# Optimization experiments

Hardware: AMD Instinct MI355X
Metric: run time of the kernel (lower is better)

The kernel has to match this reference:

```python
import jax, jax.numpy as jnp
import numpy as np
from jax import lax

B, T = 4, 2048
IN_CH, SKIP_CH, OUT_CH, K = 256, 128, 128, 5
N_MAMBA, D_STATE, D_CONV, EXPAND = 2, 16, 4, 2
D_INNER = EXPAND * OUT_CH
DT_RANK = (OUT_CH + 15) // 16  # ceil(d_model/16) = 8
L = 2 * T
EPS = 1e-5


def setup_inputs() -> dict:
    key = jax.random.key(0)
    ks = jax.random.split(key, 16)
    def rn(k, shape, s=0.02):
        return jax.random.normal(k, shape, jnp.float32) * s
    A_init = jnp.broadcast_to(jnp.arange(1, D_STATE + 1, dtype=jnp.float32),
                              (N_MAMBA, 2, D_INNER, D_STATE))
    return {
        'x': rn(ks[0], (B, IN_CH, T), 1.0),
        'skip': rn(ks[1], (B, SKIP_CH, L), 1.0),
        'up_w': rn(ks[2], (IN_CH, IN_CH, K)),       # torch ConvTranspose1d weight (in,out,k)
        'up_b': jnp.zeros((IN_CH,), jnp.float32),
        'fus_w': rn(ks[3], (OUT_CH, IN_CH + SKIP_CH)),  # 1x1 conv
        'fus_b': jnp.zeros((OUT_CH,), jnp.float32),
        'gn_w': jnp.ones((OUT_CH,), jnp.float32),
        'gn_b': jnp.zeros((OUT_CH,), jnp.float32),
        'prelu_a': jnp.array(0.25, jnp.float32),
        'ln_w': jnp.ones((N_MAMBA, OUT_CH), jnp.float32),
        'ln_b': jnp.zeros((N_MAMBA, OUT_CH), jnp.float32),
        'in_w': rn(ks[4], (N_MAMBA, 2, 2 * D_INNER, OUT_CH)),
        'conv_w': rn(ks[5], (N_MAMBA, 2, D_INNER, D_CONV), 0.1),
        'conv_b': jnp.zeros((N_MAMBA, 2, D_INNER), jnp.float32),
        'xproj_w': rn(ks[6], (N_MAMBA, 2, DT_RANK + 2 * D_STATE, D_INNER)),
        'dtproj_w': rn(ks[7], (N_MAMBA, 2, D_INNER, DT_RANK), 0.1),
        'dtproj_b': rn(ks[8], (N_MAMBA, 2, D_INNER), 0.1),
        'A_log': jnp.log(A_init),
        'Dp': jnp.ones((N_MAMBA, 2, D_INNER), jnp.float32),
        'out_w': rn(ks[9], (N_MAMBA, 2, OUT_CH, D_INNER)),
    }


def _mamba_branch(xn, cw, cb, iw, xw, dw, db, Alog, Dp, ow):
    # xn: [B, L, d_model] -> [B, L, d_model]; standard Mamba selective scan.
    xz = jnp.einsum('bld,ed->ble', xn, iw)            # [B,L,2*D_INNER]
    xi, z = jnp.split(xz, 2, axis=-1)
    # causal depthwise conv over time
    xc = lax.conv_general_dilated(xi.transpose(0, 2, 1), cw[:, None, :], (1,),
                                  [(D_CONV - 1, 0)], feature_group_count=D_INNER,
                                  dimension_numbers=('NCH', 'OIH', 'NCH'))
    xi = jax.nn.silu(xc + cb[None, :, None]).transpose(0, 2, 1)  # [B,L,D_INNER]
    dbl = jnp.einsum('bld,ed->ble', xi, xw)           # [B,L,DT_RANK+2N]
    dt = jax.nn.softplus(jnp.einsum('blr,dr->bld', dbl[..., :DT_RANK], dw) + db)
    Bc = dbl[..., DT_RANK:DT_RANK + D_STATE]          # [B,L,N]
    Cc = dbl[..., DT_RANK + D_STATE:]                 # [B,L,N]
    A = -jnp.exp(Alog)                                # [D_INNER,N]
    dA = jnp.exp(dt[..., None] * A)                   # [B,L,D_INNER,N]
    dBx = dt[..., None] * Bc[:, :, None, :] * xi[..., None]
    def comb(c1, c2):
        a1, b1 = c1
        a2, b2 = c2
        return a1 * a2, a2 * b1 + b2
    _, h = lax.associative_scan(comb, (dA, dBx), axis=1)  # h_t = dA_t h_{t-1} + dBx_t
    y = jnp.einsum('bldn,bln->bld', h, Cc) + Dp * xi
    return jnp.einsum('ble,de->bld', y * jax.nn.silu(z), ow)


def _forward(x, skip, up_w, up_b, fus_w, fus_b, gn_w, gn_b, prelu_a, ln_w, ln_b,
             in_w, conv_w, conv_b, xproj_w, dtproj_w, dtproj_b, A_log, Dp, out_w):
    p = K // 2
    # ConvTranspose1d(stride=2, padding=p, output_padding=1) == lhs-dilated conv with flipped kernel
    wt = jnp.flip(up_w, -1).transpose(1, 0, 2)        # (out,in,k)
    u = lax.conv_general_dilated(x, wt, (1,), [(K - 1 - p, K - 1 - p + 1)],
                                 lhs_dilation=(2,),
                                 dimension_numbers=('NCH', 'OIH', 'NCH'))
    u = u + up_b[None, :, None]
    u = u[..., :skip.shape[-1]]
    h = jnp.concatenate([u, skip], axis=1)            # [B, in+skip, L]
    h = jnp.einsum('bct,oc->bot', h, fus_w) + fus_b[None, :, None]
    # GroupNorm(1, C): normalize over (C,T) per sample
    mu = h.mean(axis=(1, 2), keepdims=True)
    var = h.var(axis=(1, 2), keepdims=True)
    h = (h - mu) / jnp.sqrt(var + EPS) * gn_w[None, :, None] + gn_b[None, :, None]
    h = jnp.where(h >= 0, h, prelu_a * h)             # PReLU (single param)
    h = h.transpose(0, 2, 1)                          # [B, L, C]
    for i in range(N_MAMBA):
        # BiMambaBlock: pre-LN, forward + time-reversed Mamba, residual sum
        mu2 = h.mean(-1, keepdims=True)
        v2 = h.var(-1, keepdims=True)
        xn = (h - mu2) / jnp.sqrt(v2 + EPS) * ln_w[i] + ln_b[i]
        f = _mamba_branch(xn, conv_w[i, 0], conv_b[i, 0], in_w[i, 0], xproj_w[i, 0],
                          dtproj_w[i, 0], dtproj_b[i, 0], A_log[i, 0], Dp[i, 0], out_w[i, 0])
        b = _mamba_branch(jnp.flip(xn, 1), conv_w[i, 1], conv_b[i, 1], in_w[i, 1], xproj_w[i, 1],
                          dtproj_w[i, 1], dtproj_b[i, 1], A_log[i, 1], Dp[i, 1], out_w[i, 1])
        h = h + f + jnp.flip(b, 1)
    return h.transpose(0, 2, 1)                       # [B, C_out, L]


def reference(x, skip, up_w, up_b, fus_w, fus_b, gn_w, gn_b, prelu_a, ln_w, ln_b,
              in_w, conv_w, conv_b, xproj_w, dtproj_w, dtproj_b, A_log, Dp, out_w):
    return _forward(x, skip, up_w, up_b, fus_w, fus_b, gn_w, gn_b, prelu_a, ln_w, ln_b,
                    in_w, conv_w, conv_b, xproj_w, dtproj_w, dtproj_b, A_log, Dp, out_w)
```

## Files before the change

### kernel.cpp

```cpp
#include <hip/hip_runtime.h>
#include <hip/hip_bf16.h>

#define Bsz 4
#define Tt 2048
#define Ll 4096
#define NC 256
#define CH 16
#define NG 16

typedef short bf16x8 __attribute__((ext_vector_type(8)));
typedef float f32x4 __attribute__((ext_vector_type(4)));
typedef float f32x2 __attribute__((ext_vector_type(2)));

static __device__ __forceinline__ f32x2 pk_fma(f32x2 a, f32x2 b, f32x2 c){
  f32x2 d;
  asm("v_pk_fma_f32 %0, %1, %2, %3" : "=v"(d) : "v"(a), "v"(b), "v"(c));
  return d;
}
static __device__ __forceinline__ f32x2 pk_mul(f32x2 a, f32x2 b){
  f32x2 d;
  asm("v_pk_mul_f32 %0, %1, %2" : "=v"(d) : "v"(a), "v"(b));
  return d;
}
static __device__ __forceinline__ f32x2 lo2(f32x4 v){ return (f32x2){v.x, v.y}; }
static __device__ __forceinline__ f32x2 hi2(f32x4 v){ return (f32x2){v.z, v.w}; }

static __device__ __forceinline__ float bs2f(unsigned short u){
  union{float f; unsigned int i;} v; v.i = ((unsigned int)u)<<16; return v.f;
}
static __device__ __forceinline__ unsigned short f2bs(float f){
  union{float f; unsigned int i;} v; v.f = f;
  unsigned int r = (v.i + 0x7fffu + ((v.i>>16)&1u)) >> 16;
  return (unsigned short)r;
}
static __device__ __forceinline__ unsigned short f2h(float f){
  union{_Float16 h; unsigned short u;} v; v.h = (_Float16)f; return v.u;
}
static __device__ __forceinline__ float h2f(unsigned short u){
  union{_Float16 h; unsigned short u;} v; v.u = u; return (float)v.h;
}

__global__ void k_cvt2(const float* __restrict__ a, const float* __restrict__ b,
                       unsigned short* __restrict__ da, unsigned short* __restrict__ db,
                       int na, int nb){
  int i = blockIdx.x*256 + threadIdx.x;
  if (i < na) da[i] = f2bs(a[i]);
  else {
    int j = i - na;
    if (j < nb) db[j] = f2bs(b[j]);
  }
}

__global__ void k_prepx(const float* __restrict__ xw, unsigned short* __restrict__ wxb){
  int row = blockIdx.x, br = blockIdx.y, col = threadIdx.x;
  float v = (row < 40) ? xw[((size_t)br*40 + row)*256 + col] : 0.f;
  wxb[((size_t)br*64 + row)*256 + col] = f2bs(v);
}

__global__ void k_prepA(const float* __restrict__ Alog, float* __restrict__ AEX,
                        float* __restrict__ A0C, float* __restrict__ CHN){
  int br = blockIdx.x, d = threadIdx.x;
  float A[16];
  #pragma unroll
  for (int j=0;j<4;j++){
    float4 a4 = *(const float4*)&Alog[(size_t)br*4096 + d*16 + j*4];
    A[4*j]  = -__expf(a4.x); A[4*j+1] = -__expf(a4.y);
    A[4*j+2]= -__expf(a4.z); A[4*j+3] = -__expf(a4.w);
    *(float4*)&AEX[(size_t)br*4096 + d*16 + j*4] = (float4){A[4*j],A[4*j+1],A[4*j+2],A[4*j+3]};
  }
  bool chain = true;
  #pragma unroll
  for (int n=1;n<16;n++){
    float expect = A[0]*(float)(n+1);
    if (fabsf(A[n]-expect) > 1e-3f*fabsf(expect)) chain = false;
  }
  A0C[br*256 + d] = A[0];
  CHN[br*256 + d] = chain ? 1.f : 0.f;
}

__global__ void k_compose(const float* __restrict__ up_w, const float* __restrict__ fus_w,
                          const float* __restrict__ fus_b, const float* __restrict__ up_b,
                          unsigned short* __restrict__ WEb, unsigned short* __restrict__ WOb,
                          unsigned short* __restrict__ FWSb, float* __restrict__ BIAS2){
  int i = blockIdx.x;
  int o = threadIdx.x;
  float a0=0.f,a1=0.f,a2=0.f,a3=0.f,a4=0.f;
  for (int c=0;c<256;c++){
    float f = fus_w[o*384+c];
    const float* w = up_w + ((size_t)i*256+c)*5;
    a0 += f*w[0]; a1 += f*w[1]; a2 += f*w[2];
    a3 += f*w[3]; a4 += f*w[4];
  }
  WEb[(size_t)o*768 +       i] = f2bs(a4);
  WEb[(size_t)o*768 + 256 + i] = f2bs(a2);
  WEb[(size_t)o*768 + 512 + i] = f2bs(a0);
  WOb[(size_t)o*512 +       i] = f2bs(a3);
  WOb[(size_t)o*512 + 256 + i] = f2bs(a1);
  if (i<128) FWSb[o*128 + i] = f2bs(fus_w[o*384+256+i]);
  if (i==0){
    float bb = fus_b[o];
    for (int c=0;c<256;c++) bb += fus_w[o*384+c]*up_b[c];
    BIAS2[o]=bb;
  }
}

__global__ __launch_bounds__(256) void k_tx(const float* __restrict__ x, unsigned short* __restrict__ XT){
  __shared__ float tile[64][65];
  int b=blockIdx.z, t0=blockIdx.x*64, i0=blockIdx.y*64;
  int tid=threadIdx.x;
  if (blockIdx.x==0 && blockIdx.y==0){
    XT[((size_t)b*2050)*256 + tid] = 0;
    XT[((size_t)b*2050+2049)*256 + tid] = 0;
  }
  for (int it=0;it<16;it++){
    int idx=it*256+tid; int ii=idx>>6, tt=idx&63;
    tile[ii][tt] = x[((size_t)b*256+i0+ii)*Tt + t0+tt];
  }
  __syncthreads();
  for (int it=0;it<16;it++){
    int idx=it*256+tid; int tt=idx>>6, ii=idx&63;
    XT[((size_t)b*2050 + t0+tt+1)*256 + i0+ii] = f2bs(tile[ii][tt]);
  }
}

__global__ __launch_bounds__(256) void k_ts(const float* __restrict__ skip, unsigned short* __restrict__ SKT){
  __shared__ float tile[64][65];
  int b=blockIdx.z, l0=blockIdx.x*64, s0=blockIdx.y*64;
  int tid=threadIdx.x;
  for (int it=0;it<16;it++){
    int idx=it*256+tid; int ss=idx>>6, ll=idx&63;
    tile[ss][ll] = skip[((size_t)b*128+s0+ss)*Ll + l0+ll];
  }
  __syncthreads();
  for (int it=0;it<16;it++){
    int idx=it*256+tid; int ll=idx>>6, ss=idx&63;
    SKT[((size_t)b*Ll + l0+ll)*128 + s0+ss] = f2bs(tile[ss][ll]);
  }
}

__global__ __launch_bounds__(256) void k_up(const unsigned short* __restrict__ XT,
                     const unsigned short* __restrict__ SKT,
                     const unsigned short* __restrict__ WEb, const unsigned short* __restrict__ WOb,
                     const unsigned short* __restrict__ FWSb, const float* __restrict__ B2,
                     float* __restrict__ h0, float* __restrict__ gst){
  __shared__ unsigned short XL[66*264];
  __shared__ unsigned short Wb[128*72];
  __shared__ float red0[256], red1[256];
  int bt = blockIdx.x, par = blockIdx.y, b = blockIdx.z;
  int t0 = bt*64;
  int tid = threadIdx.x;
  int wave = tid>>6, lane = tid&63;
  int wm = wave>>1, wn = wave&1;
  int quad = lane>>4, l16 = lane&15;

  for (int idx=tid; idx<66*32; idx+=256){
    int row = idx>>5, c8 = idx&31;
    *(uint4*)&XL[row*264 + c8*8] = *(const uint4*)&XT[((size_t)b*2050 + t0 + row)*256 + c8*8];
  }

  const unsigned short* Wsrc = par ? WOb : WEb;
  const int Kw = par ? 512 : 768;
  const int tapbase = par ? 1 : 0;
  f32x4 acc[2][4];
  #pragma unroll
  for (int i=0;i<2;i++)
    #pragma unroll
    for (int j=0;j<4;j++) acc[i][j] = (f32x4){0.f,0.f,0.f,0.f};

  int nch = Kw>>6;
  for (int kc=0; kc<nch; kc++){
    __syncthreads();
    #pragma unroll
    for (int it=0; it<4; it++){
      int idx = it*256+tid;
      int row = idx>>3, c8 = idx&7;
      *(uint4*)&Wb[row*72 + c8*8] = *(const uint4*)&Wsrc[(size_t)row*Kw + kc*64 + c8*8];
    }
    __syncthreads();
    #pragma unroll
    for (int ks=0; ks<64; ks+=32){
      int kg = kc*64 + ks;
      int tap = kg>>8, ib = kg&255;
      bf16x8 af[2], bf[4];
      #pragma unroll
      for (int mt=0;mt<2;mt++)
        af[mt] = *(bf16x8*)&XL[(wm*32+mt*16+l16 + tapbase + tap)*264 + ib + quad*8];
      #pragma unroll
      for (int nt=0;nt<4;nt++)
        bf[nt] = *(bf16x8*)&Wb[(wn*64+nt*16+l16)*72 + ks + quad*8];
      #pragma unroll
      for (int mt=0;mt<2;mt++)
        #pragma unroll
        for (int nt=0;nt<4;nt++)
          acc[mt][nt] = __builtin_amdgcn_mfma_f32_16x16x32_bf16(af[mt], bf[nt], acc[mt][nt], 0,0,0);
    }
  }

  __syncthreads();
  for (int idx=tid; idx<64*16; idx+=256){
    int row = idx>>4, c8 = idx&15;
    *(uint4*)&XL[row*136 + c8*8] = *(const uint4*)&SKT[((size_t)b*Ll + 2*(t0+row)+par)*128 + c8*8];
  }
  for (int kc=0; kc<2; kc++){
    __syncthreads();
    #pragma unroll
    for (int it=0; it<4; it++){
      int idx = it*256+tid;
      int row = idx>>3, c8 = idx&7;
      *(uint4*)&Wb[row*72 + c8*8] = *(const uint4*)&FWSb[(size_t)row*128 + kc*64 + c8*8];
    }
    __syncthreads();
    #pragma unroll
    for (int ks=0; ks<64; ks+=32){
      bf16x8 af[2], bf[4];
      #pragma unroll
      for (int mt=0;mt<2;mt++)
        af[mt] = *(bf16x8*)&XL[(wm*32+mt*16+l16)*136 + kc*64 + ks + quad*8];
      #pragma unroll
      for (int nt=0;nt<4;nt++)
        bf[nt] = *(bf16x8*)&Wb[(wn*64+nt*16+l16)*72 + ks + quad*8];
      #pragma unroll
      for (int mt=0;mt<2;mt++)
        #pragma unroll
        for (int nt=0;nt<4;nt++)
          acc[mt][nt] = __builtin_amdgcn_mfma_f32_16x16x32_bf16(af[mt], bf[nt], acc[mt][nt], 0,0,0);
    }
  }

  float s1=0.f, s2=0.f;
  #pragma unroll
  for (int mt=0;mt<2;mt++)
    #pragma unroll
    for (int nt=0;nt<4;nt++)
      #pragma unroll
      for (int r=0;r<4;r++){
        int m = wm*32 + mt*16 + quad*4 + r;
        int lrow = 2*(t0+m) + par;
        int col = wn*64 + nt*16 + l16;
        float v = acc[mt][nt][r] + B2[col];
        h0[((size_t)b*Ll + lrow)*128 + col] = v;
        s1 += v; s2 += v*v;
      }
  red0[tid]=s1; red1[tid]=s2;
  __syncthreads();
  for (int st=128; st>0; st>>=1){
    if (tid<st){ red0[tid]+=red0[tid+st]; red1[tid]+=red1[tid+st]; }
    __syncthreads();
  }
  if (tid==0){ atomicAdd(&gst[b*2], red0[0]); atomicAdd(&gst[b*2+1], red1[0]); }
}

__global__ __launch_bounds__(256) void k_gnln(const float* __restrict__ h0, const float* __restrict__ gn_w,
                      const float* __restrict__ gn_b, const float* __restrict__ pa,
                      const float* __restrict__ gst, const float* __restrict__ lnw,
                      const float* __restrict__ lnb, float* __restrict__ hres,
                      unsigned short* __restrict__ xn){
  int row = blockIdx.x*4 + (threadIdx.x>>6);
  int lane = threadIdx.x & 63;
  int b = row >> 12;
  const float ninv = 1.f/((float)Ll*128.f);
  float mu_g = gst[b*2]*ninv;
  float var_g = gst[b*2+1]*ninv - mu_g*mu_g;
  float inv_g = rsqrtf(var_g + 1e-5f);
  float a = pa[0];
  const float* hp = h0 + (size_t)row*128;
  float u0 = (hp[lane]   -mu_g)*inv_g*gn_w[lane]    + gn_b[lane];
  float u1 = (hp[lane+64]-mu_g)*inv_g*gn_w[lane+64] + gn_b[lane+64];
  float v0 = u0>=0.f ? u0 : a*u0;
  float v1 = u1>=0.f ? u1 : a*u1;
  float* rp = hres + (size_t)row*128;
  rp[lane] = v0; rp[lane+64] = v1;
  float s = v0+v1, q = v0*v0+v1*v1;
  #pragma unroll
  for (int off=32; off>0; off>>=1){
    s += __shfl_xor(s, off, 64);
    q += __shfl_xor(q, off, 64);
  }
  float mu = s*(1.f/128.f);
  float rs = rsqrtf(q*(1.f/128.f)-mu*mu + 1e-5f);
  unsigned short* xp = xn + (size_t)row*128;
  xp[lane]    = f2bs((v0-mu)*rs*lnw[lane]    + lnb[lane]);
  xp[lane+64] = f2bs((v1-mu)*rs*lnw[lane+64] + lnb[lane+64]);
}

__global__ __launch_bounds__(256) void k_gemm_in(const unsigned short* __restrict__ A,
                          const unsigned short* __restrict__ W,
                          unsigned short* __restrict__ C){
  __shared__ unsigned short As[128*72];
  __shared__ unsigned short Bs[128*72];
  int tid = threadIdx.x;
  int row0 = blockIdx.x*128;
  int n0   = blockIdx.y*128;
  int dir  = blockIdx.z;
  const unsigned short* Wp = W + (size_t)dir*512*128;
  unsigned short* Cp = C + (size_t)dir*Bsz*Ll*512;
  int wave = tid>>6, lane = tid&63;
  int wm = wave>>1, wn = wave&1;
  int quad = lane>>4, l16 = lane&15;
  f32x4 acc[4][4];
  #pragma unroll
  for (int i=0;i<4;i++)
    #pragma unroll
    for (int j=0;j<4;j++) acc[i][j] = (f32x4){0.f,0.f,0.f,0.f};

  for (int kb=0; kb<128; kb+=64){
    __syncthreads();
    #pragma unroll
    for (int it=0; it<4; it++){
      int idx = it*256 + tid;
      int row = idx>>3, c8 = idx&7;
      int r = row0 + row;
      int p = r & (Ll-1); int bb = r >> 12;
      int src = (bb<<12) + (dir ? (Ll-1-p) : p);
      *(uint4*)&As[row*72 + c8*8] = *(const uint4*)&A[(size_t)src*128 + kb + c8*8];
      *(uint4*)&Bs[row*72 + c8*8] = *(const uint4*)&Wp[(size_t)(n0+row)*128 + kb + c8*8];
    }
    __syncthreads();
    #pragma unroll
    for (int ks=0; ks<64; ks+=32){
      bf16x8 af[4], bf[4];
      #pragma unroll
      for (int mt=0;mt<4;mt++)
        af[mt] = *(bf16x8*)&As[(wm*64+mt*16+l16)*72 + ks + quad*8];
      #pragma unroll
      for (int nt=0;nt<4;nt++)
        bf[nt] = *(bf16x8*)&Bs[(wn*64+nt*16+l16)*72 + ks + quad*8];
      #pragma unroll
      for (int mt=0;mt<4;mt++)
        #pragma unroll
        for (int nt=0;nt<4;nt++)
          acc[mt][nt] = __builtin_amdgcn_mfma_f32_16x16x32_bf16(af[mt], bf[nt], acc[mt][nt], 0,0,0);
    }
  }
  #pragma unroll
  for (int mt=0;mt<4;mt++)
    #pragma unroll
    for (int nt=0;nt<4;nt++)
      #pragma unroll
      for (int r=0;r<4;r++){
        int row = row0 + wm*64 + mt*16 + quad*4 + r;
        int col = n0 + wn*64 + nt*16 + l16;
        Cp[(size_t)row*512 + col] = f2bs(acc[mt][nt][r]);
      }
}

template<int DO_LN>
__global__ __launch_bounds__(256) void k_gemm_out_t(const unsigned short* __restrict__ Y,
                           const unsigned short* __restrict__ W,
                           float* __restrict__ C, const float* __restrict__ lnw,
                           const float* __restrict__ lnb, unsigned short* __restrict__ xn){
  __shared__ unsigned short As[64*72];
  __shared__ unsigned short Bs[128*72];
  __shared__ float redS[2][4][2][4][2][2];
  int tid = threadIdx.x;
  int row0 = blockIdx.x*64;
  int wave = tid>>6, lane = tid&63;
  int wm = wave>>1, wn = wave&1;
  int quad = lane>>4, l16 = lane&15;
  const size_t planeY = (size_t)Bsz*Ll*256;
  f32x4 acc[2][4];
  #pragma unroll
  for (int i=0;i<2;i++)
    #pragma unroll
    for (int j=0;j<4;j++) acc[i][j] = (f32x4){0.f,0.f,0.f,0.f};

  for (int kc=0; kc<8; kc++){
    int dirp = kc>>2;
    int kb = (kc&3)*64;
    const unsigned short* Wp = W + (size_t)dirp*128*256;
    __syncthreads();
    #pragma unroll
    for (int it=0; it<2; it++){
      int idx = it*256 + tid;
      int row = idx>>3, c8 = idx&7;
      int r = row0 + row;
      int p = r & (Ll-1); int bb = r >> 12;
      int srow = dirp ? ((bb<<12) + (Ll-1-p)) : r;
      *(uint4*)&As[row*72 + c8*8] = *(const uint4*)&Y[dirp*planeY + (size_t)srow*256 + kb + c8*8];
    }
    #pragma unroll
    for (int it=0; it<4; it++){
      int idx = it*256 + tid;
      int row = idx>>3, c8 = idx&7;
      *(uint4*)&Bs[row*72 + c8*8] = *(const uint4*)&Wp[(size_t)row*256 + kb + c8*8];
    }
    __syncthreads();
    #pragma unroll
    for (int ks=0; ks<64; ks+=32){
      bf16x8 af[2], bf[4];
      #pragma unroll
      for (int mt=0;mt<2;mt++)
        af[mt] = *(bf16x8*)&As[(wm*32+mt*16+l16)*72 + ks + quad*8];
      #pragma unroll
      for (int nt=0;nt<4;nt++)
        bf[nt] = *(bf16x8*)&Bs[(wn*64+nt*16+l16)*72 + ks + quad*8];
      #pragma unroll
      for (int mt=0;mt<2;mt++)
        #pragma unroll
        for (int nt=0;nt<4;nt++)
          acc[mt][nt] = __builtin_amdgcn_mfma_f32_16x16x32_bf16(af[mt], bf[nt], acc[mt][nt], 0,0,0);
    }
  }

  float vals[2][4][4];
  #pragma unroll
  for (int mt=0;mt<2;mt++)
    #pragma unroll
    for (int nt=0;nt<4;nt++)
      #pragma unroll
      for (int r=0;r<4;r++){
        int row = row0 + wm*32 + mt*16 + quad*4 + r;
        int col = wn*64 + nt*16 + l16;
        float v = C[(size_t)row*128 + col] + acc[mt][nt][r];
        C[(size_t)row*128 + col] = v;
        vals[mt][nt][r] = v;
      }

  if (DO_LN){
    #pragma unroll
    for (int mt=0;mt<2;mt++)
      #pragma unroll
      for (int r=0;r<4;r++){
        float s = 0.f, q = 0.f;
        #pragma unroll
        for (int nt=0;nt<4;nt++){ float v = vals[mt][nt][r]; s += v; q += v*v; }
        #pragma unroll
        for (int off=1; off<16; off<<=1){
          s += __shfl_xor(s, off, 64);
          q += __shfl_xor(q, off, 64);
        }
        if (l16 == 0){
          redS[wm][quad][mt][r][wn][0] = s;
          redS[wm][quad][mt][r][wn][1] = q;
        }
      }
    __syncthreads();
    #pragma unroll
    for (int mt=0;mt<2;mt++)
      #pragma unroll
      for (int r=0;r<4;r++){
        float s = redS[wm][quad][mt][r][0][0] + redS[wm][quad][mt][r][1][0];
        float q = redS[wm][quad][mt][r][0][1] + redS[wm][quad][mt][r][1][1];
        float mu = s*(1.f/128.f);
        float rs = rsqrtf(q*(1.f/128.f) - mu*mu + 1e-5f);
        int row = row0 + wm*32 + mt*16 + quad*4 + r;
        #pragma unroll
        for (int nt=0;nt<4;nt++){
          int col = wn*64 + nt*16 + l16;
          xn[(size_t)row*128 + col] = f2bs((vals[mt][nt][r]-mu)*rs*lnw[col] + lnb[col]);
        }
      }
  }
}

__global__ __launch_bounds__(256) void k_xproj3(const unsigned short* __restrict__ xz,
                        const unsigned short* __restrict__ wxb,
                        const float* __restrict__ cw, const float* __restrict__ cb,
                        unsigned short* __restrict__ xib, float* __restrict__ dbl){
  __shared__ unsigned short xiS[64*264];
  __shared__ unsigned short Bs[64*72];
  int tid = threadIdx.x;
  int dir = blockIdx.y;
  xz  += (size_t)dir*Bsz*Ll*512;
  wxb += (size_t)dir*64*256;
  cw  += dir*1024;
  cb  += dir*256;
  xib += (size_t)dir*Bsz*Ll*256;
  dbl += (size_t)dir*Bsz*Ll*40;
  size_t row0 = (size_t)blockIdx.x*64;
  int p0 = (int)(row0 & (Ll-1));

  {
    int d = tid;
    float4 w4 = *(const float4*)&cw[d*4];
    float bias = cb[d];
    float w0, w1, w2;
    if (p0 == 0){ w0=0.f; w1=0.f; w2=0.f; }
    else {
      w0 = bs2f(xz[(row0-3)*512 + d]);
      w1 = bs2f(xz[(row0-2)*512 + d]);
      w2 = bs2f(xz[(row0-1)*512 + d]);
    }
    #pragma unroll 4
    for (int rr=0; rr<64; rr++){
      float xv = bs2f(xz[(row0+rr)*512 + d]);
      float acc = bias + w4.x*w0 + w4.y*w1 + w4.z*w2 + w4.w*xv;
      float v = acc*__builtin_amdgcn_rcpf(1.f+__expf(-acc));
      unsigned short us = f2bs(v);
      xiS[rr*264 + d] = us;
      xib[(row0+rr)*256 + d] = us;
      w0=w1; w1=w2; w2=xv;
    }
  }

  int wave = tid>>6, lane = tid&63;
  int quad = lane>>4, l16 = lane&15;
  f32x4 acc[4];
  #pragma unroll
  for (int j=0;j<4;j++) acc[j] = (f32x4){0.f,0.f,0.f,0.f};

  for (int kb=0; kb<256; kb+=64){
    __syncthreads();
    #pragma unroll
    for (int it=0; it<2; it++){
      int idx = it*256 + tid;
      int row = idx>>3, c8 = idx&7;
      *(uint4*)&Bs[row*72 + c8*8] = *(const uint4*)&wxb[(size_t)row*256 + kb + c8*8];
    }
    __syncthreads();
    #pragma unroll
    for (int ks=0; ks<64; ks+=32){
      bf16x8 af = *(bf16x8*)&xiS[(wave*16+l16)*264 + kb + ks + quad*8];
      #pragma unroll
      for (int nt=0;nt<4;nt++){
        bf16x8 bf = *(bf16x8*)&Bs[(nt*16+l16)*72 + ks + quad*8];
        acc[nt] = __builtin_amdgcn_mfma_f32_16x16x32_bf16(af, bf, acc[nt], 0,0,0);
      }
    }
  }
  #pragma unroll
  for (int nt=0;nt<4;nt++)
    #pragma unroll
    for (int r=0;r<4;r++){
      int m = wave*16 + quad*4 + r;
      int col = nt*16 + l16;
      if (col < 40) dbl[(row0+m)*40 + col] = acc[nt][r];
    }
}

#define POWTREE2(e1, pw2) { \
  float _e2 = (e1)*(e1); \
  f32x2 _e2v = (f32x2){_e2,_e2}; \
  pw2[0] = (f32x2){(e1),_e2}; \
  pw2[1] = pk_mul(pw2[0], _e2v); \
  pw2[2] = pk_mul(pw2[1], _e2v); \
  pw2[3] = pk_mul(pw2[2], _e2v); \
  f32x2 _e8v = (f32x2){pw2[3].y, pw2[3].y}; \
  pw2[4] = pk_mul(pw2[0], _e8v); \
  pw2[5] = pk_mul(pw2[1], _e8v); \
  pw2[6] = pk_mul(pw2[2], _e8v); \
  pw2[7] = pk_mul(pw2[3], _e8v); }

__global__ __launch_bounds__(256) void k_scan1(const float* __restrict__ dbl,
                       const unsigned short* __restrict__ xib,
                       unsigned short* __restrict__ xz,
                       const float* __restrict__ AEX,
                       const float* __restrict__ A0C, const float* __restrict__ CHNf,
                       const float* __restrict__ dtw, const float* __restrict__ dtb,
                       float* __restrict__ SD, float* __restrict__ Q){
  __shared__ float dblS[CH*24];
  int b = blockIdx.y, c = blockIdx.x, dir = blockIdx.z;
  int d = threadIdx.x;
  const float* dblP = dbl + (size_t)dir*Bsz*Ll*40;
  const unsigned short* xiP = xib + (size_t)dir*Bsz*Ll*256;
  unsigned short* xzP = xz + (size_t)dir*Bsz*Ll*512;
  size_t base = (size_t)b*Ll + (size_t)c*CH;
  if (d < CH*6){
    int p = d/6, j = d - p*6;
    *(float4*)&dblS[p*24 + j*4] = *(const float4*)&dblP[(base+p)*40 + j*4];
  }
  float A0 = A0C[dir*256 + d];
  bool chain = CHNf[dir*256 + d] != 0.f;
  f32x2 wv2[4];
  {
    const float* dw = dtw + (size_t)dir*2048 + d*8;
    float4 w0 = *(const float4*)&dw[0];
    float4 w1 = *(const float4*)&dw[4];
    wv2[0]=(f32x2){w0.x,w0.y}; wv2[1]=(f32x2){w0.z,w0.w};
    wv2[2]=(f32x2){w1.x,w1.y}; wv2[3]=(f32x2){w1.z,w1.w};
  }
  float bbt = dtb[dir*256 + d];
  __syncthreads();
  float sdt = 0.f;
  const unsigned short* xip = xiP + base*256 + d;
  unsigned short* dtp = xzP + base*512 + d;
  size_t sbase = (size_t)dir*Bsz*NC*4096 + ((size_t)(b*NC + c))*4096 + (size_t)d*16;
  if (chain){
    bool n1 = fabsf(A0 + 1.f) < 1e-6f;
    float xv[CH];
    #pragma unroll
    for (int p=0;p<CH;p++) xv[p] = bs2f(xip[(size_t)p*256]);
    f32x2 h2[8];
    #pragma unroll
    for (int i=0;i<8;i++) h2[i] = (f32x2){0.f,0.f};
    #pragma unroll
    for (int p=0;p<CH;p++){
      const float* rw = &dblS[p*24];
      f32x4 t0 = *(const f32x4*)&rw[0];
      f32x4 t1 = *(const f32x4*)&rw[4];
      f32x2 dp = pk_mul(lo2(t0), wv2[0]);
      dp = pk_fma(hi2(t0), wv2[1], dp);
      dp = pk_fma(lo2(t1), wv2[2], dp);
      dp = pk_fma(hi2(t1), wv2[3], dp);
      float a0 = bbt + dp.x + dp.y;
      float t = __expf(a0);
      float u = 1.f + t;
      float dtv = (a0>20.f)? a0 : __logf(u);
      float e1 = n1 ? __builtin_amdgcn_rcpf(u) : __expf(dtv*A0);
      dtp[(size_t)p*512] = f2h(dtv);
      float dx = dtv*xv[p];
      sdt += dtv;
      f32x2 pw2[8];
      POWTREE2(e1, pw2);
      f32x2 dxv = (f32x2){dx,dx};
      f32x4 b0 = *(const f32x4*)&dblS[p*24+8];
      f32x4 b1 = *(const f32x4*)&dblS[p*24+12];
      f32x4 b2 = *(const f32x4*)&dblS[p*24+16];
      f32x4 b3 = *(const f32x4*)&dblS[p*24+20];
      h2[0] = pk_fma(pw2[0], h2[0], pk_mul(lo2(b0), dxv));
      h2[1] = pk_fma(pw2[1], h2[1], pk_mul(hi2(b0), dxv));
      h2[2] = pk_fma(pw2[2], h2[2], pk_mul(lo2(b1), dxv));
      h2[3] = pk_fma(pw2[3], h2[3], pk_mul(hi2(b1), dxv));
      h2[4] = pk_fma(pw2[4], h2[4], pk_mul(lo2(b2), dxv));
      h2[5] = pk_fma(pw2[5], h2[5], pk_mul(hi2(b2), dxv));
      h2[6] = pk_fma(pw2[6], h2[6], pk_mul(lo2(b3), dxv));
      h2[7] = pk_fma(pw2[7], h2[7], pk_mul(hi2(b3), dxv));
    }
    #pragma unroll
    for (int j=0;j<4;j++)
      *(float4*)&Q[sbase + 4*j] = (float4){h2[2*j].x,h2[2*j].y,h2[2*j+1].x,h2[2*j+1].y};
  } else {
    float A[16];
    #pragma unroll
    for (int j=0;j<4;j++)
      *(float4*)&A[4*j] = *(const float4*)&AEX[(size_t)dir*4096 + d*16 + j*4];
    float h[16];
    #pragma unroll
    for (int n=0;n<16;n++) h[n]=0.f;
    for (int p=0;p<CH;p++){
      const float* rw = &dblS[p*24];
      float4 t0 = *(const float4*)&rw[0], t1 = *(const float4*)&rw[4];
      float a0 = bbt + t0.x*wv2[0].x+t0.y*wv2[0].y+t0.z*wv2[1].x+t0.w*wv2[1].y
                     + t1.x*wv2[2].x+t1.y*wv2[2].y+t1.z*wv2[3].x+t1.w*wv2[3].y;
      float dtv = (a0>20.f)? a0 : __logf(1.f+__expf(a0));
      dtp[(size_t)p*512] = f2h(dtv);
      float xiv = bs2f(xip[(size_t)p*256]);
      float dx = dtv*xiv;
      sdt += dtv;
      float bc[16];
      *(float4*)&bc[0]  = *(const float4*)&rw[8];
      *(float4*)&bc[4]  = *(const float4*)&rw[12];
      *(float4*)&bc[8]  = *(const float4*)&rw[16];
      *(float4*)&bc[12] = *(const float4*)&rw[20];
      #pragma unroll
      for (int n=0;n<16;n++){
        float a = __expf(dtv*A[n]);
        h[n] = a*h[n] + bc[n]*dx;
      }
    }
    #pragma unroll
    for (int j=0;j<4;j++)
      *(float4*)&Q[sbase + 4*j] = (float4){h[4*j],h[4*j+1],h[4*j+2],h[4*j+3]};
  }
  SD[(((size_t)dir*Bsz + b)*NC + c)*256 + d] = sdt;
}

__global__ __launch_bounds__(64) void k_scan2a(float* __restrict__ SD, float* __restrict__ Q,
                        float* __restrict__ SDG, float* __restrict__ QG,
                        const float* __restrict__ AEX){
  int zb = blockIdx.z;
  int dir = zb >> 2;
  int g  = blockIdx.y;
  int t  = blockIdx.x*64 + threadIdx.x;
  int dn4 = t*4;
  int d = dn4 >> 4;
  float4 A4 = *(const float4*)&AEX[(size_t)dir*4096 + dn4];
  float* sd = SD + (((size_t)zb*NC) + (size_t)g*(NC/NG))*256 + d;
  float* q  = Q + (size_t)zb*NC*4096 + (size_t)g*(NC/NG)*4096 + dn4;
  float4 H = {0.f,0.f,0.f,0.f};
  float S = 0.f;
  #pragma unroll
  for (int c2=0; c2<NC/NG; c2++){
    float s_c = sd[(size_t)c2*256];
    float4 q_c = *(const float4*)(q + (size_t)c2*4096);
    sd[(size_t)c2*256] = S;
    *(float4*)(q + (size_t)c2*4096) = H;
    float4 p;
    p.x = __expf(A4.x*s_c); p.y = __expf(A4.y*s_c);
    p.z = __expf(A4.z*s_c); p.w = __expf(A4.w*s_c);
    H.x = p.x*H.x + q_c.x; H.y = p.y*H.y + q_c.y;
    H.z = p.z*H.z + q_c.z; H.w = p.w*H.w + q_c.w;
    S += s_c;
  }
  SDG[((size_t)zb*NG + g)*256 + d] = S;
  *(float4*)&QG[((size_t)zb*NG + g)*4096 + dn4] = H;
}

__global__ __launch_bounds__(64) void k_scan2b(const float* __restrict__ SDG, float* __restrict__ QG,
                        const float* __restrict__ AEX){
  int b = blockIdx.y, dir = blockIdx.z;
  int zb = dir*Bsz + b;
  int t = blockIdx.x*64 + threadIdx.x;
  int dn4 = t*4;
  int d = dn4 >> 4;
  float4 A4 = *(const float4*)&AEX[(size_t)dir*4096 + dn4];
  const float* sg = SDG + (size_t)zb*NG*256 + d;
  float* qg = QG + (size_t)zb*NG*4096 + dn4;
  float4 H = {0.f,0.f,0.f,0.f};
  #pragma unroll
  for (int g=0; g<NG; g++){
    float s = sg[(size_t)g*256];
    float4 qe = *(const float4*)(qg + (size_t)g*4096);
    *(float4*)(qg + (size_t)g*4096) = H;
    float4 p;
    p.x = __expf(A4.x*s); p.y = __expf(A4.y*s);
    p.z = __expf(A4.z*s); p.w = __expf(A4.w*s);
    H.x = p.x*H.x + qe.x; H.y = p.y*H.y + qe.y;
    H.z = p.z*H.z + qe.z; H.w = p.w*H.w + qe.w;
  }
}

__global__ __launch_bounds__(256) void k_scan3(const float* __restrict__ dbl,
                       unsigned short* xiy, const float* __restrict__ AEX,
                       const float* __restrict__ A0C, const float* __restrict__ CHNf,
                       const float* __restrict__ Dpw, const float* __restrict__ Hs,
                       const float* __restrict__ SDp, const float* __restrict__ QG,
                       const unsigned short* __restrict__ xz){
  __shared__ float dblS[CH*32];
  int b = blockIdx.y, c = blockIdx.x, dir = blockIdx.z;
  int d = threadIdx.x;
  const float* dblP = dbl + (size_t)dir*Bsz*Ll*40;
  unsigned short* xiP = xiy + (size_t)dir*Bsz*Ll*256;
  const unsigned short* xzP = xz + (size_t)dir*Bsz*Ll*512;
  size_t base = (size_t)b*Ll + (size_t)c*CH;
  if (d < CH*8){
    int p = d>>3, j = d&7;
    *(float4*)&dblS[p*32 + j*4] = *(const float4*)&dblP[(base+p)*40 + 8 + j*4];
  }
  float A0 = A0C[dir*256 + d];
  bool chain = CHNf[dir*256 + d] != 0.f;
  float Dp = Dpw[dir*256 + d];
  int zb = dir*Bsz + b;
  size_t sbase = (size_t)zb*NC*4096 + (size_t)c*4096 + (size_t)d*16;
  float sdtp = SDp[(((size_t)zb)*NC + c)*256 + d];
  size_t gbase = ((size_t)zb*NG + (c >> 4))*4096 + (size_t)d*16;
  __syncthreads();
  unsigned short* xip = xiP + base*256 + d;
  const unsigned short* dtp = xzP + base*512 + d;
  const unsigned short* zp  = xzP + base*512 + 256 + d;
  if (chain){
    float xv[CH], zv[CH], dv[CH];
    #pragma unroll
    for (int p=0;p<CH;p++) xv[p] = bs2f(xip[(size_t)p*256]);
    #pragma unroll
    for (int p=0;p<CH;p++) zv[p] = bs2f(zp[(size_t)p*512]);
    #pragma unroll
    for (int p=0;p<CH;p++) dv[p] = h2f(dtp[(size_t)p*512]);
    f32x2 h2[8];
    {
      float eg = __expf(A0*sdtp);
      f32x2 pg[8];
      POWTREE2(eg, pg);
      #pragma unroll
      for (int j=0;j<4;j++){
        float4 h4 = *(const float4*)&Hs[sbase + 4*j];
        float4 g4 = *(const float4*)&QG[gbase + 4*j];
        h2[2*j]   = pk_fma(pg[2*j],   (f32x2){g4.x,g4.y}, (f32x2){h4.x,h4.y});
        h2[2*j+1] = pk_fma(pg[2*j+1], (f32x2){g4.z,g4.w}, (f32x2){h4.z,h4.w});
      }
    }
    #pragma unroll
    for (int p=0;p<CH;p++){
      const float* rw = &dblS[p*32];
      float dtv = dv[p];
      float e1 = __expf(dtv*A0);
      float dx = dtv*xv[p];
      f32x2 pw2[8];
      POWTREE2(e1, pw2);
      f32x2 dxv = (f32x2){dx,dx};
      f32x4 b0 = *(const f32x4*)&rw[0];
      f32x4 b1 = *(const f32x4*)&rw[4];
      f32x4 b2 = *(const f32x4*)&rw[8];
      f32x4 b3 = *(const f32x4*)&rw[12];
      f32x4 c0 = *(const f32x4*)&rw[16];
      f32x4 c1 = *(const f32x4*)&rw[20];
      f32x4 c2 = *(const f32x4*)&rw[24];
      f32x4 c3 = *(const f32x4*)&rw[28];
      f32x2 ya;
      h2[0] = pk_fma(pw2[0], h2[0], pk_mul(lo2(b0), dxv));
      ya = pk_mul(h2[0], lo2(c0));
      h2[1] = pk_fma(pw2[1], h2[1], pk_mul(hi2(b0), dxv));
      ya = pk_fma(h2[1], hi2(c0), ya);
      h2[2] = pk_fma(pw2[2], h2[2], pk_mul(lo2(b1), dxv));
      ya = pk_fma(h2[2], lo2(c1), ya);
      h2[3] = pk_fma(pw2[3], h2[3], pk_mul(hi2(b1), dxv));
      ya = pk_fma(h2[3], hi2(c1), ya);
      h2[4] = pk_fma(pw2[4], h2[4], pk_mul(lo2(b2), dxv));
      ya = pk_fma(h2[4], lo2(c2), ya);
      h2[5] = pk_fma(pw2[5], h2[5], pk_mul(hi2(b2), dxv));
      ya = pk_fma(h2[5], hi2(c2), ya);
      h2[6] = pk_fma(pw2[6], h2[6], pk_mul(lo2(b3), dxv));
      ya = pk_fma(h2[6], lo2(c3), ya);
      h2[7] = pk_fma(pw2[7], h2[7], pk_mul(hi2(b3), dxv));
      ya = pk_fma(h2[7], hi2(c3), ya);
      float acc = ya.x + ya.y;
      float z = zv[p];
      float g = z*__builtin_amdgcn_rcpf(1.f+__expf(-z));
      xip[(size_t)p*256] = f2bs((acc + Dp*xv[p])*g);
    }
  } else {
    float A[16];
    #pragma unroll
    for (int j=0;j<4;j++)
      *(float4*)&A[4*j] = *(const float4*)&AEX[(size_t)dir*4096 + d*16 + j*4];
    float h[16];
    #pragma unroll
    for (int j=0;j<4;j++){
      float4 h4 = *(const float4*)&Hs[sbase + 4*j];
      float4 g4 = *(const float4*)&QG[gbase + 4*j];
      h[4*j]   = __expf(A[4*j]*sdtp)*g4.x   + h4.x;
      h[4*j+1] = __expf(A[4*j+1]*sdtp)*g4.y + h4.y;
      h[4*j+2] = __expf(A[4*j+2]*sdtp)*g4.z + h4.z;
      h[4*j+3] = __expf(A[4*j+3]*sdtp)*g4.w + h4.w;
    }
    for (int p=0;p<CH;p++){
      const float* rw = &dblS[p*32];
      float dtv = h2f(dtp[(size_t)p*512]);
      float xiv = bs2f(xip[(size_t)p*256]);
      float dx = dtv*xiv;
      float bc[16], cc[16];
      *(float4*)&bc[0]  = *(const float4*)&rw[0];
      *(float4*)&bc[4]  = *(const float4*)&rw[4];
      *(float4*)&bc[8]  = *(const float4*)&rw[8];
      *(float4*)&bc[12] = *(const float4*)&rw[12];
      *(float4*)&cc[0]  = *(const float4*)&rw[16];
      *(float4*)&cc[4]  = *(const float4*)&rw[20];
      *(float4*)&cc[8]  = *(const float4*)&rw[24];
      *(float4*)&cc[12] = *(const float4*)&rw[28];
      float acc = 0.f;
      #pragma unroll
      for (int n=0;n<16;n++){
        float a = __expf(dtv*A[n]);
        h[n] = a*h[n] + bc[n]*dx;
        acc += h[n]*cc[n];
      }
      float z = bs2f(zp[(size_t)p*512]);
      float g = z*__builtin_amdgcn_rcpf(1.f+__expf(-z));
      xip[(size_t)p*256] = f2bs((acc + Dp*xiv)*g);
    }
  }
}

__global__ __launch_bounds__(256) void k_final(const float* __restrict__ hres, float* __restrict__ out){
  __shared__ float tile[64*129];
  int b = blockIdx.y, l0 = blockIdx.x*64;
  int tid = threadIdx.x;
  for (int q=0;q<32;q++){
    int idx = q*256 + tid;
    int l = idx >> 7, c = idx & 127;
    tile[l*129 + c] = hres[((size_t)b*Ll + l0 + l)*128 + c];
  }
  __syncthreads();
  int lo = tid & 63; int cbase = tid >> 6;
  for (int q=0;q<32;q++){
    int c = cbase + q*4;
    out[((size_t)b*128 + c)*Ll + l0 + lo] = tile[lo*129 + c];
  }
}

extern "C" void kernel_launch(void* const* d_in, const int* in_sizes, int n_in,
                              void* d_out, int out_size, void* d_ws, size_t ws_size,
                              hipStream_t stream){
  const float* x      = (const float*)d_in[0];
  const float* skip   = (const float*)d_in[1];
  const float* up_w   = (const float*)d_in[2];
  const float* up_b   = (const float*)d_in[3];
  const float* fus_w  = (const float*)d_in[4];
  const float* fus_b  = (const float*)d_in[5];
  const float* gn_w   = (const float*)d_in[6];
  const float* gn_b   = (const float*)d_in[7];
  const float* pa     = (const float*)d_in[8];
  const float* ln_w   = (const float*)d_in[9];
  const float* ln_b   = (const float*)d_in[10];
  const float* in_w   = (const float*)d_in[11];
  const float* conv_w = (const float*)d_in[12];
  const float* conv_b = (const float*)d_in[13];
  const float* xproj_w= (const float*)d_in[14];
  const float* dtproj_w=(const float*)d_in[15];
  const float* dtproj_b=(const float*)d_in[16];
  const float* A_log  = (const float*)d_in[17];
  const float* Dp     = (const float*)d_in[18];
  const float* out_w  = (const float*)d_in[19];

  float* w = (float*)d_ws;
  size_t off=0;
  float* B2 = w+off; off += 128;
  float* GST= w+off; off += 16;
  off = (off+3)&~(size_t)3;
  float* HR = w+off; off += (size_t)Bsz*Ll*128;
  float* DBL2= w+off; off += 2*(size_t)Bsz*Ll*40;
  unsigned short* XNB = (unsigned short*)(w+off); off += (size_t)Bsz*Ll*128/2;
  unsigned short* XZB2= (unsigned short*)(w+off); off += 2*(size_t)Bsz*Ll*512/2;
  unsigned short* IWB = (unsigned short*)(w+off); off += 2*2*512*128/2;
  unsigned short* OWB = (unsigned short*)(w+off); off += 2*2*128*256/2;
  unsigned short* WXB = (unsigned short*)(w+off); off += 2*2*64*256/2;
  unsigned short* WEb = (unsigned short*)(w+off); off += 768*128/2;
  unsigned short* WOb = (unsigned short*)(w+off); off += 512*128/2;
  unsigned short* FWSb= (unsigned short*)(w+off); off += 128*128/2;
  float* AEXb = w+off; off += 4*4096;
  float* A0Cb = w+off; off += 4*256;
  float* CHNb = w+off; off += 4*256;
  float* SDGb = w+off; off += (size_t)2*Bsz*NG*256;
  size_t planeS = (size_t)Bsz*NC*4096;
  float* U1 = w+off; off += 2*planeS;
  unsigned short* XT  = (unsigned short*)U1;
  unsigned short* SKT = (unsigned short*)(U1 + 1049604);
  float* SQ = U1;
  float* SD = (float*)XNB;
  float* QG = SD + 524288;
  float* U2 = w+off; off += 2*(size_t)Bsz*Ll*128;
  float* H0 = U2;
  unsigned short* XIB2 = (unsigned short*)U2;

  hipMemsetAsync(GST, 0, 16*sizeof(float), stream);
  k_cvt2<<<(2*2*512*128 + 2*2*128*256 + 255)/256,256,0,stream>>>(in_w, out_w, IWB, OWB,
                                                                 2*2*512*128, 2*2*128*256);
  k_prepx<<<dim3(64,4),256,0,stream>>>(xproj_w, WXB);
  k_prepA<<<4,256,0,stream>>>(A_log, AEXb, A0Cb, CHNb);
  k_compose<<<256,128,0,stream>>>(up_w, fus_w, fus_b, up_b, WEb, WOb, FWSb, B2);
  k_tx<<<dim3(Tt/64, 4, Bsz),256,0,stream>>>(x, XT);
  k_ts<<<dim3(Ll/64, 2, Bsz),256,0,stream>>>(skip, SKT);
  k_up<<<dim3(32, 2, Bsz),256,0,stream>>>(XT, SKT, WEb, WOb, FWSb, B2, H0, GST);
  k_gnln<<<Bsz*Ll/4,256,0,stream>>>(H0, gn_w, gn_b, pa, GST, ln_w, ln_b, HR, XNB);
  for (int i=0;i<2;i++){
    k_gemm_in<<<dim3(128,4,2),256,0,stream>>>(XNB, IWB + (size_t)(i*2)*512*128, XZB2);
    k_xproj3<<<dim3(Bsz*Ll/64,2),256,0,stream>>>(XZB2, WXB + (size_t)(i*2)*64*256,
                                                 conv_w + (i*2)*1024, conv_b + (i*2)*256,
                                                 XIB2, DBL2);
    k_scan1<<<dim3(NC,Bsz,2),256,0,stream>>>(DBL2, XIB2, XZB2, AEXb + (size_t)(i*2)*4096,
                                             A0Cb + (i*2)*256, CHNb + (i*2)*256,
                                             dtproj_w + (i*2)*2048, dtproj_b + (i*2)*256, SD, SQ);
    k_scan2a<<<dim3(16,NG,2*Bsz),64,0,stream>>>(SD, SQ, SDGb, QG, AEXb + (size_t)(i*2)*4096);
    k_scan2b<<<dim3(16,Bsz,2),64,0,stream>>>(SDGb, QG, AEXb + (size_t)(i*2)*4096);
    k_scan3<<<dim3(NC,Bsz,2),256,0,stream>>>(DBL2, XIB2, AEXb + (size_t)(i*2)*4096,
                                             A0Cb + (i*2)*256, CHNb + (i*2)*256,
                                             Dp + (i*2)*256, SQ, SD, QG, XZB2);
    if (i==0)
      k_gemm_out_t<1><<<256,256,0,stream>>>(XIB2, OWB + 0, HR, ln_w + 128, ln_b + 128, XNB);
    else
      k_gemm_out_t<0><<<256,256,0,stream>>>(XIB2, OWB + (size_t)2*128*256, HR,
                                            (const float*)nullptr, (const float*)nullptr,
                                            (unsigned short*)nullptr);
  }
  k_final<<<dim3(Ll/64,Bsz),256,0,stream>>>(HR, (float*)d_out);
}
```

Measured before the change: 383.6 us.

## Merge weight-prep kernels into one launch and halve k_up time tile

Five small preprocessing steps (two weight conversions, x-proj padding, A-table prep and the GroupNorm-stats memset) become one kernel that dispatches by block index, removing several launches and a memset. k_up now tiles 32 time steps per block instead of 64, doubling the grid from 256 to 512 blocks to fill more CUs. The cost is less weight reuse per block and twice as many weight loads and atomics.

```diff
diff --git a/kernel.cpp b/kernel.cpp
--- a/kernel.cpp
+++ b/kernel.cpp
@@ -40,67 +40,69 @@
   union{_Float16 h; unsigned short u;} v; v.u = u; return (float)v.h;
 }
 
-__global__ void k_cvt2(const float* __restrict__ a, const float* __restrict__ b,
-                       unsigned short* __restrict__ da, unsigned short* __restrict__ db,
-                       int na, int nb){
-  int i = blockIdx.x*256 + threadIdx.x;
-  if (i < na) da[i] = f2bs(a[i]);
-  else {
-    int j = i - na;
-    if (j < nb) db[j] = f2bs(b[j]);
-  }
-}
-
-__global__ void k_prepx(const float* __restrict__ xw, unsigned short* __restrict__ wxb){
-  int row = blockIdx.x, br = blockIdx.y, col = threadIdx.x;
-  float v = (row < 40) ? xw[((size_t)br*40 + row)*256 + col] : 0.f;
-  wxb[((size_t)br*64 + row)*256 + col] = f2bs(v);
-}
-
-__global__ void k_prepA(const float* __restrict__ Alog, float* __restrict__ AEX,
-                        float* __restrict__ A0C, float* __restrict__ CHN){
-  int br = blockIdx.x, d = threadIdx.x;
-  float A[16];
-  #pragma unroll
-  for (int j=0;j<4;j++){
-    float4 a4 = *(const float4*)&Alog[(size_t)br*4096 + d*16 + j*4];
-    A[4*j]  = -__expf(a4.x); A[4*j+1] = -__expf(a4.y);
-    A[4*j+2]= -__expf(a4.z); A[4*j+3] = -__expf(a4.w);
-    *(float4*)&AEX[(size_t)br*4096 + d*16 + j*4] = (float4){A[4*j],A[4*j+1],A[4*j+2],A[4*j+3]};
-  }
-  bool chain = true;
-  #pragma unroll
-  for (int n=1;n<16;n++){
-    float expect = A[0]*(float)(n+1);
-    if (fabsf(A[n]-expect) > 1e-3f*fabsf(expect)) chain = false;
-  }
-  A0C[br*256 + d] = A[0];
-  CHN[br*256 + d] = chain ? 1.f : 0.f;
-}
-
-__global__ void k_compose(const float* __restrict__ up_w, const float* __restrict__ fus_w,
-                          const float* __restrict__ fus_b, const float* __restrict__ up_b,
-                          unsigned short* __restrict__ WEb, unsigned short* __restrict__ WOb,
-                          unsigned short* __restrict__ FWSb, float* __restrict__ BIAS2){
-  int i = blockIdx.x;
-  int o = threadIdx.x;
-  float a0=0.f,a1=0.f,a2=0.f,a3=0.f,a4=0.f;
-  for (int c=0;c<256;c++){
-    float f = fus_w[o*384+c];
-    const float* w = up_w + ((size_t)i*256+c)*5;
-    a0 += f*w[0]; a1 += f*w[1]; a2 += f*w[2];
-    a3 += f*w[3]; a4 += f*w[4];
-  }
-  WEb[(size_t)o*768 +       i] = f2bs(a4);
-  WEb[(size_t)o*768 + 256 + i] = f2bs(a2);
-  WEb[(size_t)o*768 + 512 + i] = f2bs(a0);
-  WOb[(size_t)o*512 +       i] = f2bs(a3);
-  WOb[(size_t)o*512 + 256 + i] = f2bs(a1);
-  if (i<128) FWSb[o*128 + i] = f2bs(fus_w[o*384+256+i]);
-  if (i==0){
-    float bb = fus_b[o];
-    for (int c=0;c<256;c++) bb += fus_w[o*384+c]*up_b[c];
-    BIAS2[o]=bb;
+__global__ __launch_bounds__(256) void k_prep(
+    const float* __restrict__ in_w, const float* __restrict__ out_w,
+    unsigned short* __restrict__ IWB, unsigned short* __restrict__ OWB,
+    const float* __restrict__ xw, unsigned short* __restrict__ wxb,
+    const float* __restrict__ Alog, float* __restrict__ AEX,
+    float* __restrict__ A0C, float* __restrict__ CHN, float* __restrict__ GST,
+    const float* __restrict__ up_w, const float* __restrict__ fus_w,
+    const float* __restrict__ fus_b, const float* __restrict__ up_b,
+    unsigned short* __restrict__ WEb, unsigned short* __restrict__ WOb,
+    unsigned short* __restrict__ FWSb, float* __restrict__ BIAS2){
+  const int na = 2*2*512*128;
+  const int nb = 2*2*128*256;
+  int bid = blockIdx.x, tid = threadIdx.x;
+  if (bid < 3072){
+    int i = bid*256 + tid;
+    if (i < na) IWB[i] = f2bs(in_w[i]);
+    else { int j = i - na; if (j < nb) OWB[j] = f2bs(out_w[j]); }
+  } else if (bid < 3328){
+    int r = bid - 3072;
+    int row = r & 63, br = r >> 6;
+    float v = (row < 40) ? xw[((size_t)br*40 + row)*256 + tid] : 0.f;
+    wxb[((size_t)br*64 + row)*256 + tid] = f2bs(v);
+  } else if (bid < 3332){
+    int br = bid - 3328, d = tid;
+    float A[16];
+    #pragma unroll
+    for (int j=0;j<4;j++){
+      float4 a4 = *(const float4*)&Alog[(size_t)br*4096 + d*16 + j*4];
+      A[4*j]  = -__expf(a4.x); A[4*j+1] = -__expf(a4.y);
+      A[4*j+2]= -__expf(a4.z); A[4*j+3] = -__expf(a4.w);
+      *(float4*)&AEX[(size_t)br*4096 + d*16 + j*4] = (float4){A[4*j],A[4*j+1],A[4*j+2],A[4*j+3]};
+    }
+    bool chain = true;
+    #pragma unroll
+    for (int n=1;n<16;n++){
+      float expect = A[0]*(float)(n+1);
+      if (fabsf(A[n]-expect) > 1e-3f*fabsf(expect)) chain = false;
+    }
+    A0C[br*256 + d] = A[0];
+    CHN[br*256 + d] = chain ? 1.f : 0.f;
+    if (br==0 && d<16) GST[d] = 0.f;
+  } else {
+    int r = bid - 3332;
+    int i = r*2 + (tid>>7);
+    int o = tid & 127;
+    float a0=0.f,a1=0.f,a2=0.f,a3=0.f,a4=0.f;
+    for (int c=0;c<256;c++){
+      float f = fus_w[o*384+c];
+      const float* w = up_w + ((size_t)i*256+c)*5;
+      a0 += f*w[0]; a1 += f*w[1]; a2 += f*w[2];
+      a3 += f*w[3]; a4 += f*w[4];
+    }
+    WEb[(size_t)o*768 +       i] = f2bs(a4);
+    WEb[(size_t)o*768 + 256 + i] = f2bs(a2);
+    WEb[(size_t)o*768 + 512 + i] = f2bs(a0);
+    WOb[(size_t)o*512 +       i] = f2bs(a3);
+    WOb[(size_t)o*512 + 256 + i] = f2bs(a1);
+    if (i<128) FWSb[o*128 + i] = f2bs(fus_w[o*384+256+i]);
+    if (i==0){
+      float bb = fus_b[o];
+      for (int c=0;c<256;c++) bb += fus_w[o*384+c]*up_b[c];
+      BIAS2[o]=bb;
+    }
   }
 }
 
@@ -143,17 +145,17 @@
                      const unsigned short* __restrict__ WEb, const unsigned short* __restrict__ WOb,
                      const unsigned short* __restrict__ FWSb, const float* __restrict__ B2,
                      float* __restrict__ h0, float* __restrict__ gst){
-  __shared__ unsigned short XL[66*264];
+  __shared__ unsigned short XL[34*264];
   __shared__ unsigned short Wb[128*72];
   __shared__ float red0[256], red1[256];
   int bt = blockIdx.x, par = blockIdx.y, b = blockIdx.z;
-  int t0 = bt*64;
+  int t0 = bt*32;
   int tid = threadIdx.x;
   int wave = tid>>6, lane = tid&63;
   int wm = wave>>1, wn = wave&1;
   int quad = lane>>4, l16 = lane&15;
 
-  for (int idx=tid; idx<66*32; idx+=256){
+  for (int idx=tid; idx<34*32; idx+=256){
     int row = idx>>5, c8 = idx&31;
     *(uint4*)&XL[row*264 + c8*8] = *(const uint4*)&XT[((size_t)b*2050 + t0 + row)*256 + c8*8];
   }
@@ -161,11 +163,9 @@
   const unsigned short* Wsrc = par ? WOb : WEb;
   const int Kw = par ? 512 : 768;
   const int tapbase = par ? 1 : 0;
-  f32x4 acc[2][4];
-  #pragma unroll
-  for (int i=0;i<2;i++)
-    #pragma unroll
-    for (int j=0;j<4;j++) acc[i][j] = (f32x4){0.f,0.f,0.f,0.f};
+  f32x4 acc[4];
+  #pragma unroll
+  for (int j=0;j<4;j++) acc[j] = (f32x4){0.f,0.f,0.f,0.f};
 
   int nch = Kw>>6;
   for (int kc=0; kc<nch; kc++){
@@ -181,23 +181,17 @@
     for (int ks=0; ks<64; ks+=32){
       int kg = kc*64 + ks;
       int tap = kg>>8, ib = kg&255;
-      bf16x8 af[2], bf[4];
-      #pragma unroll
-      for (int mt=0;mt<2;mt++)
-        af[mt] = *(bf16x8*)&XL[(wm*32+mt*16+l16 + tapbase + tap)*264 + ib + quad*8];
-      #pragma unroll
-      for (int nt=0;nt<4;nt++)
-        bf[nt] = *(bf16x8*)&Wb[(wn*64+nt*16+l16)*72 + ks + quad*8];
-      #pragma unroll
-      for (int mt=0;mt<2;mt++)
-        #pragma unroll
-        for (int nt=0;nt<4;nt++)
-          acc[mt][nt] = __builtin_amdgcn_mfma_f32_16x16x32_bf16(af[mt], bf[nt], acc[mt][nt], 0,0,0);
+      bf16x8 af = *(bf16x8*)&XL[(wm*16+l16 + tapbase + tap)*264 + ib + quad*8];
+      #pragma unroll
+      for (int nt=0;nt<4;nt++){
+        bf16x8 bf = *(bf16x8*)&Wb[(wn*64+nt*16+l16)*72 + ks + quad*8];
+        acc[nt] = __builtin_amdgcn_mfma_f32_16x16x32_bf16(af, bf, acc[nt], 0,0,0);
+      }
     }
   }
 
   __syncthreads();
-  for (int idx=tid; idx<64*16; idx+=256){
+  for (int idx=tid; idx<32*16; idx+=256){
     int row = idx>>4, c8 = idx&15;
     *(uint4*)&XL[row*136 + c8*8] = *(const uint4*)&SKT[((size_t)b*Ll + 2*(t0+row)+par)*128 + c8*8];
   }
@@ -212,35 +206,27 @@
     __syncthreads();
     #pragma unroll
     for (int ks=0; ks<64; ks+=32){
-      bf16x8 af[2], bf[4];
-      #pragma unroll
-      for (int mt=0;mt<2;mt++)
-        af[mt] = *(bf16x8*)&XL[(wm*32+mt*16+l16)*136 + kc*64 + ks + quad*8];
-      #pragma unroll
-      for (int nt=0;nt<4;nt++)
-        bf[nt] = *(bf16x8*)&Wb[(wn*64+nt*16+l16)*72 + ks + quad*8];
-      #pragma unroll
-      for (int mt=0;mt<2;mt++)
-        #pragma unroll
-        for (int nt=0;nt<4;nt++)
-          acc[mt][nt] = __builtin_amdgcn_mfma_f32_16x16x32_bf16(af[mt], bf[nt], acc[mt][nt], 0,0,0);
+      bf16x8 af = *(bf16x8*)&XL[(wm*16+l16)*136 + kc*64 + ks + quad*8];
+      #pragma unroll
+      for (int nt=0;nt<4;nt++){
+        bf16x8 bf = *(bf16x8*)&Wb[(wn*64+nt*16+l16)*72 + ks + quad*8];
+        acc[nt] = __builtin_amdgcn_mfma_f32_16x16x32_bf16(af, bf, acc[nt], 0,0,0);
+      }
     }
   }
 
   float s1=0.f, s2=0.f;
   #pragma unroll
-  for (int mt=0;mt<2;mt++)
-    #pragma unroll
-    for (int nt=0;nt<4;nt++)
-      #pragma unroll
-      for (int r=0;r<4;r++){
-        int m = wm*32 + mt*16 + quad*4 + r;
-        int lrow = 2*(t0+m) + par;
-        int col = wn*64 + nt*16 + l16;
-        float v = acc[mt][nt][r] + B2[col];
-        h0[((size_t)b*Ll + lrow)*128 + col] = v;
-        s1 += v; s2 += v*v;
-      }
+  for (int nt=0;nt<4;nt++)
+    #pragma unroll
+    for (int r=0;r<4;r++){
+      int m = wm*16 + quad*4 + r;
+      int lrow = 2*(t0+m) + par;
+      int col = wn*64 + nt*16 + l16;
+      float v = acc[nt][r] + B2[col];
+      h0[((size_t)b*Ll + lrow)*128 + col] = v;
+      s1 += v; s2 += v*v;
+    }
   red0[tid]=s1; red1[tid]=s2;
   __syncthreads();
   for (int st=128; st>0; st>>=1){
@@ -912,15 +898,13 @@
   float* H0 = U2;
   unsigned short* XIB2 = (unsigned short*)U2;
 
-  hipMemsetAsync(GST, 0, 16*sizeof(float), stream);
-  k_cvt2<<<(2*2*512*128 + 2*2*128*256 + 255)/256,256,0,stream>>>(in_w, out_w, IWB, OWB,
-                                                                 2*2*512*128, 2*2*128*256);
-  k_prepx<<<dim3(64,4),256,0,stream>>>(xproj_w, WXB);
-  k_prepA<<<4,256,0,stream>>>(A_log, AEXb, A0Cb, CHNb);
-  k_compose<<<256,128,0,stream>>>(up_w, fus_w, fus_b, up_b, WEb, WOb, FWSb, B2);
+  k_prep<<<3460,256,0,stream>>>(in_w, out_w, IWB, OWB,
+                                xproj_w, WXB,
+                                A_log, AEXb, A0Cb, CHNb, GST,
+                                up_w, fus_w, fus_b, up_b, WEb, WOb, FWSb, B2);
   k_tx<<<dim3(Tt/64, 4, Bsz),256,0,stream>>>(x, XT);
   k_ts<<<dim3(Ll/64, 2, Bsz),256,0,stream>>>(skip, SKT);
-  k_up<<<dim3(32, 2, Bsz),256,0,stream>>>(XT, SKT, WEb, WOb, FWSb, B2, H0, GST);
+  k_up<<<dim3(Tt/32, 2, Bsz),256,0,stream>>>(XT, SKT, WEb, WOb, FWSb, B2, H0, GST);
   k_gnln<<<Bsz*Ll/4,256,0,stream>>>(H0, gn_w, gn_b, pa, GST, ln_w, ln_b, HR, XNB);
   for (int i=0;i<2;i++){
     k_gemm_in<<<dim3(128,4,2),256,0,stream>>>(XNB, IWB + (size_t)(i*2)*512*128, XZB2);
```

Measured after the change: 390.7 us. No clear change (+1.9%).
